# Kernel optimization log

Hardware: AMD Instinct MI355X
Metric: run time of the kernel (lower is better)

## Reference

```python
import jax, jax.numpy as jnp
import numpy as np

B, S, V, D, H, DK, DH, L = 1, 2048, 256, 1024, 16, 64, 4096, 4
EPS = 1e-5
SCALE = 1.0 / np.sqrt(DK)


def _ln(x, g, b):
    mu = jnp.mean(x, axis=-1, keepdims=True)
    var = jnp.mean(jnp.square(x - mu), axis=-1, keepdims=True)
    return (x - mu) * jax.lax.rsqrt(var + EPS) * g + b


def setup_inputs() -> dict:
    key = jax.random.key(0)
    ks = jax.random.split(key, 20)
    f = lambda k, shape: (0.02 * jax.random.normal(k, shape)).astype(jnp.float32)
    return {
        "x": jax.random.randint(ks[0], (B, S), 0, V),
        "emb": f(ks[1], (V, D)),
        "pos": f(ks[2], (S, D)),
        "Wq": f(ks[3], (L, D, H * DK)), "bq": jnp.zeros((L, H * DK), jnp.float32),
        "Wk": f(ks[4], (L, D, H * DK)), "bk": jnp.zeros((L, H * DK), jnp.float32),
        "Wv": f(ks[5], (L, D, H * DK)), "bv": jnp.zeros((L, H * DK), jnp.float32),
        "Wo": f(ks[6], (L, H * DK, D)),
        "ln1_g": jnp.ones((L, D), jnp.float32), "ln1_b": jnp.zeros((L, D), jnp.float32),
        "W1": f(ks[7], (L, D, DH)), "b1": jnp.zeros((L, DH), jnp.float32),
        "W2": f(ks[8], (L, DH, D)), "b2": jnp.zeros((L, D), jnp.float32),
        "ln2_g": jnp.ones((L, D), jnp.float32), "ln2_b": jnp.zeros((L, D), jnp.float32),
        "head_w": f(ks[9], (D, V)), "head_b": jnp.zeros((V,), jnp.float32),
    }


def _forward(x, emb, pos, Wq, bq, Wk, bk, Wv, bv, Wo, ln1_g, ln1_b,
             W1, b1, W2, b2, ln2_g, ln2_b, head_w, head_b):
    h = emb[x] + pos[:S]                      # [B,S,D]
    causal = jnp.tril(jnp.ones((S, S), bool))  # additive -inf above diag
    for i in range(L):
        # --- naive attention: explicit QK^T, mask, softmax, @V ---
        q = (h @ Wq[i] + bq[i]).reshape(B, S, H, DK)
        k = (h @ Wk[i] + bk[i]).reshape(B, S, H, DK)
        v = (h @ Wv[i] + bv[i]).reshape(B, S, H, DK)
        scores = jnp.einsum('bqhd,bkhd->bhqk', q * SCALE, k)   # [B,H,S,S]
        scores = jnp.where(causal[None, None], scores, -jnp.inf)
        p = jax.nn.softmax(scores, axis=-1)
        a = jnp.einsum('bhqk,bkhd->bqhd', p, v).reshape(B, S, H * DK) @ Wo[i]
        # --- TransformerLayer: x + ln2(mlp(x + ln1(attn(x)))) ---
        u = h + _ln(a, ln1_g[i], ln1_b[i])
        m = jax.nn.gelu(u @ W1[i] + b1[i], approximate=False) @ W2[i] + b2[i]
        h = h + _ln(m, ln2_g[i], ln2_b[i])
    return h @ head_w + head_b                 # [B,S,V]


def reference(x, emb, pos, Wq, bq, Wk, bk, Wv, bv, Wo, ln1_g, ln1_b,
              W1, b1, W2, b2, ln2_g, ln2_b, head_w, head_b):
    return _forward(x, emb, pos, Wq, bq, Wk, bk, Wv, bv, Wo, ln1_g, ln1_b,
                    W1, b1, W2, b2, ln2_g, ln2_b, head_w, head_b)
```

## Files before the change

### kernel.cpp

```cpp
#include <hip/hip_runtime.h>
#include <hip/hip_bf16.h>
#include <cstdint>
#include <math.h>

static constexpr int S_  = 2048;
static constexpr int D_  = 1024;
static constexpr int H_  = 16;
static constexpr int DK_ = 64;
static constexpr int DH_ = 4096;
static constexpr int L_  = 4;
static constexpr int V_  = 256;
#define ATT_SCALE 0.125f

typedef __bf16 bf16;
typedef __bf16 bf16x8 __attribute__((ext_vector_type(8)));
typedef __bf16 bf16x4v __attribute__((ext_vector_type(4)));
typedef float  f32x4  __attribute__((ext_vector_type(4)));

__device__ __forceinline__ __attribute__((address_space(3))) void* to_lds(const void* p) {
  return (__attribute__((address_space(3))) void*)(uintptr_t)p;
}
__device__ __forceinline__ __attribute__((address_space(1))) void* to_glb(const void* p) {
  return (__attribute__((address_space(1))) void*)(uintptr_t)p;
}

template <int GELU_EPI>
__global__ __launch_bounds__(256) void gemm_bf16_kernel(
    const bf16* __restrict__ A, const bf16* __restrict__ Bt,
    const float* __restrict__ bias, float* __restrict__ Cf, bf16* __restrict__ Cb,
    int M, int N, int K)
{
  __shared__ __align__(16) bf16 sA[2][128 * 64];
  __shared__ __align__(16) bf16 sB[2][64 * 64];
  const int tid  = threadIdx.x;
  const int wave = tid >> 6;
  const int lane = tid & 63;
  const int l16  = lane & 15;
  const int quad = lane >> 4;
  const int bm = blockIdx.x * 128;
  const int bn = blockIdx.y * 64;
  const int wm = (wave & 1) * 64;
  const int wn = (wave >> 1) * 32;

  const int srow = tid >> 3;
  const int sc8  = (tid & 7) ^ (srow & 7);
  const bf16* gA = A  + (size_t)(bm + srow) * K + sc8 * 8;
  const bf16* gB = Bt + (size_t)(bn + srow) * K + sc8 * 8;

  const int swz = l16 & 7;

  f32x4 acc[4][2] = {};

#pragma unroll
  for (int u = 0; u < 4; ++u)
    __builtin_amdgcn_global_load_lds(to_glb(gA + (size_t)u * 32 * K),
                                     to_lds(&sA[0][u * 2048 + tid * 8]), 16, 0, 0);
#pragma unroll
  for (int u = 0; u < 2; ++u)
    __builtin_amdgcn_global_load_lds(to_glb(gB + (size_t)u * 32 * K),
                                     to_lds(&sB[0][u * 2048 + tid * 8]), 16, 0, 0);

  int cur = 0;
  for (int k0 = 0; k0 < K; k0 += 64, cur ^= 1) {
    if (k0 + 64 < K) {
      const int nb = cur ^ 1;
      const size_t ko = k0 + 64;
#pragma unroll
      for (int u = 0; u < 4; ++u)
        __builtin_amdgcn_global_load_lds(to_glb(gA + ko + (size_t)u * 32 * K),
                                         to_lds(&sA[nb][u * 2048 + tid * 8]), 16, 0, 0);
#pragma unroll
      for (int u = 0; u < 2; ++u)
        __builtin_amdgcn_global_load_lds(to_glb(gB + ko + (size_t)u * 32 * K),
                                         to_lds(&sB[nb][u * 2048 + tid * 8]), 16, 0, 0);
      asm volatile("s_waitcnt vmcnt(6)" ::: "memory");
    } else {
      asm volatile("s_waitcnt vmcnt(0)" ::: "memory");
    }
    __builtin_amdgcn_s_barrier();

    bf16x8 af[2][4], bfv[2][2];
#pragma unroll
    for (int kc = 0; kc < 2; ++kc) {
      const int c8 = ((kc * 4 + quad) ^ swz) * 8;
#pragma unroll
      for (int i = 0; i < 4; ++i)
        af[kc][i] = *(const bf16x8*)&sA[cur][(wm + i * 16 + l16) * 64 + c8];
#pragma unroll
      for (int j = 0; j < 2; ++j)
        bfv[kc][j] = *(const bf16x8*)&sB[cur][(wn + j * 16 + l16) * 64 + c8];
    }
    asm volatile("s_waitcnt lgkmcnt(0)" ::: "memory");
    __builtin_amdgcn_s_barrier();

#pragma unroll
    for (int kc = 0; kc < 2; ++kc)
#pragma unroll
      for (int i = 0; i < 4; ++i)
#pragma unroll
        for (int j = 0; j < 2; ++j)
          acc[i][j] = __builtin_amdgcn_mfma_f32_16x16x32_bf16(af[kc][i], bfv[kc][j], acc[i][j], 0, 0, 0);
  }

#pragma unroll
  for (int i = 0; i < 4; ++i) {
#pragma unroll
    for (int j = 0; j < 2; ++j) {
      const int col = bn + wn + j * 16 + l16;
      const float bz = bias ? bias[col] : 0.0f;
#pragma unroll
      for (int r = 0; r < 4; ++r) {
        const int row = bm + wm + i * 16 + quad * 4 + r;
        float v = acc[i][j][r] + bz;
        if (GELU_EPI) v = 0.5f * v * (1.0f + erff(v * 0.70710678118654752f));
        if (Cf) Cf[(size_t)row * N + col] = v;
        if (Cb) Cb[(size_t)row * N + col] = (bf16)v;
      }
    }
  }
}

__global__ __launch_bounds__(256) void transpose_cast_kernel(
    const float* __restrict__ in, bf16* __restrict__ out, int K, int N)
{
  __shared__ float t[32][33];
  const int k0 = blockIdx.y * 32;
  const int n0 = blockIdx.x * 32;
  const int tx = threadIdx.x & 31;
  const int ty = threadIdx.x >> 5;
#pragma unroll
  for (int i = 0; i < 32; i += 8)
    t[ty + i][tx] = in[(size_t)(k0 + ty + i) * N + (n0 + tx)];
  __syncthreads();
#pragma unroll
  for (int i = 0; i < 32; i += 8)
    out[(size_t)(n0 + ty + i) * K + (k0 + tx)] = (bf16)t[tx][ty + i];
}

__global__ __launch_bounds__(256) void transpose3_cast_kernel(
    const float* __restrict__ in0, const float* __restrict__ in1, const float* __restrict__ in2,
    bf16* __restrict__ out, int K, int N)
{
  const float* in = (blockIdx.z == 0) ? in0 : (blockIdx.z == 1) ? in1 : in2;
  bf16* o = out + (size_t)blockIdx.z * K * N;
  __shared__ float t[32][33];
  const int k0 = blockIdx.y * 32;
  const int n0 = blockIdx.x * 32;
  const int tx = threadIdx.x & 31;
  const int ty = threadIdx.x >> 5;
#pragma unroll
  for (int i = 0; i < 32; i += 8)
    t[ty + i][tx] = in[(size_t)(k0 + ty + i) * N + (n0 + tx)];
  __syncthreads();
#pragma unroll
  for (int i = 0; i < 32; i += 8)
    o[(size_t)(n0 + ty + i) * K + (k0 + tx)] = (bf16)t[tx][ty + i];
}

__global__ __launch_bounds__(256) void vtrans_kernel(
    const bf16* __restrict__ qkv, bf16* __restrict__ vT)
{
  __shared__ bf16 t[32][65];
  const int s0 = blockIdx.x * 32;
  const int head = blockIdx.y;
  const int sr = threadIdx.x >> 3, d8 = (threadIdx.x & 7) * 8;
  bf16x8 v = *(const bf16x8*)(qkv + (size_t)(s0 + sr) * (3 * D_) + 2 * D_ + head * DK_ + d8);
#pragma unroll
  for (int i = 0; i < 8; ++i) t[sr][d8 + i] = v[i];
  __syncthreads();
  const int dw = threadIdx.x >> 2, s4 = (threadIdx.x & 3) * 8;
  bf16x8 o;
#pragma unroll
  for (int i = 0; i < 8; ++i) o[i] = t[s4 + i][dw];
  *(bf16x8*)(vT + (size_t)head * DK_ * S_ + (size_t)dw * S_ + s0 + s4) = o;
}

__global__ __launch_bounds__(256) void embed_kernel(
    const int* __restrict__ x, const float* __restrict__ emb, const float* __restrict__ pos,
    float* __restrict__ hf, bf16* __restrict__ hb)
{
  const int s = blockIdx.x;
  const int d = threadIdx.x * 4;
  const int tok = x[s];
  const float4 e = *(const float4*)(emb + (size_t)tok * D_ + d);
  const float4 p = *(const float4*)(pos + (size_t)s * D_ + d);
  float4 o; o.x = e.x + p.x; o.y = e.y + p.y; o.z = e.z + p.z; o.w = e.w + p.w;
  *(float4*)(hf + (size_t)s * D_ + d) = o;
  bf16x4v ob = {(bf16)o.x, (bf16)o.y, (bf16)o.z, (bf16)o.w};
  *(bf16x4v*)(hb + (size_t)s * D_ + d) = ob;
}

__device__ __forceinline__ float wave_reduce_sum(float v) {
#pragma unroll
  for (int off = 32; off > 0; off >>= 1) v += __shfl_xor(v, off, 64);
  return v;
}

__global__ __launch_bounds__(256) void ln_add_kernel(
    const float* __restrict__ src, const float* __restrict__ resid,
    const float* __restrict__ g, const float* __restrict__ b,
    float* __restrict__ outf, bf16* __restrict__ outb)
{
  const int r = blockIdx.x;
  const int t = threadIdx.x;
  const float4 x = ((const float4*)(src + (size_t)r * D_))[t];
  float s  = x.x + x.y + x.z + x.w;
  float s2 = x.x * x.x + x.y * x.y + x.z * x.z + x.w * x.w;
  s  = wave_reduce_sum(s);
  s2 = wave_reduce_sum(s2);
  __shared__ float red[8];
  const int wave = t >> 6, lane = t & 63;
  if (lane == 0) { red[wave] = s; red[4 + wave] = s2; }
  __syncthreads();
  s  = red[0] + red[1] + red[2] + red[3];
  s2 = red[4] + red[5] + red[6] + red[7];
  const float mu  = s * (1.0f / 1024.0f);
  const float var = s2 * (1.0f / 1024.0f) - mu * mu;
  const float rs  = rsqrtf(var + 1e-5f);
  const float4 gv = ((const float4*)g)[t];
  const float4 bv = ((const float4*)b)[t];
  const float4 hv = ((const float4*)(resid + (size_t)r * D_))[t];
  const float o0 = hv.x + (x.x - mu) * rs * gv.x + bv.x;
  const float o1 = hv.y + (x.y - mu) * rs * gv.y + bv.y;
  const float o2 = hv.z + (x.z - mu) * rs * gv.z + bv.z;
  const float o3 = hv.w + (x.w - mu) * rs * gv.w + bv.w;
  if (outf) { float4 o4; o4.x = o0; o4.y = o1; o4.z = o2; o4.w = o3;
              ((float4*)(outf + (size_t)r * D_))[t] = o4; }
  if (outb) { bf16x4v ob = {(bf16)o0, (bf16)o1, (bf16)o2, (bf16)o3};
              ((bf16x4v*)(outb + (size_t)r * D_))[t] = ob; }
}

__global__ __launch_bounds__(256) void attn_mfma_kernel(
    const bf16* __restrict__ qkv, const bf16* __restrict__ vT, bf16* __restrict__ out)
{
  __shared__ __align__(16) bf16 sK[2][64 * 64];
  __shared__ __align__(16) bf16 sV[2][64 * 64];
  __shared__ __align__(16) bf16 sP[4][16 * 64];

  const int head = blockIdx.y;
  const int xb   = blockIdx.x;
  const int qIdx = (head & 8) ? (31 - xb) : xb;
  const int qb   = qIdx * 64;
  const int tid  = threadIdx.x;
  const int wave = tid >> 6, lane = tid & 63;
  const int l16  = lane & 15, quad = lane >> 4;
  const int swz  = l16 & 7;

  const size_t rstr = 3 * D_;
  const bf16* kbase = qkv + D_ + head * DK_;
  const bf16* vbase = vT + (size_t)head * DK_ * S_;

  const int srow   = tid >> 3;
  const int kchunk = (tid & 7) ^ (srow & 7);

  bf16x8 aq0, aq1;
  {
    const bf16* qrow = qkv + (size_t)(qb + wave * 16 + l16) * rstr + head * DK_ + quad * 8;
    bf16x8 t0 = *(const bf16x8*)(qrow);
    bf16x8 t1 = *(const bf16x8*)(qrow + 32);
#pragma unroll
    for (int i = 0; i < 8; ++i) {
      aq0[i] = (bf16)((float)t0[i] * ATT_SCALE);
      aq1[i] = (bf16)((float)t1[i] * ATT_SCALE);
    }
  }

  f32x4 oa[4] = {};
  float lsum[4] = {0.0f, 0.0f, 0.0f, 0.0f};
  const int qrow0 = qb + wave * 16 + quad * 4;
  const int jmax = qb + 63;

#pragma unroll
  for (int u = 0; u < 2; ++u) {
    const int r = u * 32 + srow;
    __builtin_amdgcn_global_load_lds(to_glb(kbase + (size_t)r * rstr + kchunk * 8),
                                     to_lds(&sK[0][u * 2048 + tid * 8]), 16, 0, 0);
    __builtin_amdgcn_global_load_lds(to_glb(vbase + (size_t)r * S_ + kchunk * 8),
                                     to_lds(&sV[0][u * 2048 + tid * 8]), 16, 0, 0);
  }

  int cur = 0;
  for (int j0 = 0; j0 <= jmax; j0 += 64, cur ^= 1) {
    if (j0 + 64 <= jmax) {
      const int nb = cur ^ 1;
      const int jn = j0 + 64;
#pragma unroll
      for (int u = 0; u < 2; ++u) {
        const int r = u * 32 + srow;
        __builtin_amdgcn_global_load_lds(to_glb(kbase + (size_t)(jn + r) * rstr + kchunk * 8),
                                         to_lds(&sK[nb][u * 2048 + tid * 8]), 16, 0, 0);
        __builtin_amdgcn_global_load_lds(to_glb(vbase + (size_t)r * S_ + jn + kchunk * 8),
                                         to_lds(&sV[nb][u * 2048 + tid * 8]), 16, 0, 0);
      }
      asm volatile("s_waitcnt vmcnt(4)" ::: "memory");
    } else {
      asm volatile("s_waitcnt vmcnt(0)" ::: "memory");
    }
    __builtin_amdgcn_s_barrier();

    f32x4 sc[4];
#pragma unroll
    for (int n = 0; n < 4; ++n) {
      const bf16* kr = &sK[cur][(n * 16 + l16) * 64];
      bf16x8 bk0 = *(const bf16x8*)(kr + ((quad    ) ^ swz) * 8);
      bf16x8 bk1 = *(const bf16x8*)(kr + ((quad + 4) ^ swz) * 8);
      f32x4 z = {};
      z = __builtin_amdgcn_mfma_f32_16x16x32_bf16(aq0, bk0, z, 0, 0, 0);
      z = __builtin_amdgcn_mfma_f32_16x16x32_bf16(aq1, bk1, z, 0, 0, 0);
      sc[n] = z;
    }
    bf16 pb[4][4];
#pragma unroll
    for (int n = 0; n < 4; ++n) {
      const int key = j0 + n * 16 + l16;
#pragma unroll
      for (int r = 0; r < 4; ++r) {
        const float p = (key <= qrow0 + r) ? __expf(sc[n][r]) : 0.0f;
        lsum[r] += p;
        pb[n][r] = (bf16)p;
      }
    }
    bf16* pw = &sP[wave][0];
    const int cb = l16 >> 3, co = l16 & 7;
#pragma unroll
    for (int n = 0; n < 4; ++n) {
#pragma unroll
      for (int r = 0; r < 4; ++r) {
        const int row = quad * 4 + r;
        const int ch = (2 * n + cb) ^ (row & 7);
        pw[row * 64 + ch * 8 + co] = pb[n][r];
      }
    }
    asm volatile("s_waitcnt lgkmcnt(0)" ::: "memory");
    __builtin_amdgcn_wave_barrier();
    bf16x8 ap0 = *(const bf16x8*)&pw[l16 * 64 + ((quad    ) ^ swz) * 8];
    bf16x8 ap1 = *(const bf16x8*)&pw[l16 * 64 + ((quad + 4) ^ swz) * 8];

#pragma unroll
    for (int n = 0; n < 4; ++n) {
      const bf16* vr = &sV[cur][(n * 16 + l16) * 64];
      bf16x8 bv0 = *(const bf16x8*)(vr + ((quad    ) ^ swz) * 8);
      bf16x8 bv1 = *(const bf16x8*)(vr + ((quad + 4) ^ swz) * 8);
      oa[n] = __builtin_amdgcn_mfma_f32_16x16x32_bf16(ap0, bv0, oa[n], 0, 0, 0);
      oa[n] = __builtin_amdgcn_mfma_f32_16x16x32_bf16(ap1, bv1, oa[n], 0, 0, 0);
    }
    asm volatile("s_waitcnt lgkmcnt(0)" ::: "memory");
    __builtin_amdgcn_s_barrier();
  }

#pragma unroll
  for (int r = 0; r < 4; ++r) {
#pragma unroll
    for (int off = 1; off <= 8; off <<= 1)
      lsum[r] += __shfl_xor(lsum[r], off, 64);
  }
#pragma unroll
  for (int r = 0; r < 4; ++r) {
    const float inv = 1.0f / lsum[r];
    const int qrow = qrow0 + r;
#pragma unroll
    for (int n = 0; n < 4; ++n)
      out[(size_t)qrow * D_ + head * DK_ + n * 16 + l16] = (bf16)(oa[n][r] * inv);
  }
}

__global__ __launch_bounds__(256) void pack3_kernel(
    const float* __restrict__ a, const float* __restrict__ b, const float* __restrict__ c,
    float* __restrict__ out)
{
  const int i = blockIdx.x * 256 + threadIdx.x;
  if (i < 1024) out[i] = a[i];
  else if (i < 2048) out[i] = b[i - 1024];
  else if (i < 3072) out[i] = c[i - 2048];
}

extern "C" void kernel_launch(void* const* d_in, const int* in_sizes, int n_in,
                              void* d_out, int out_size, void* d_ws, size_t ws_size,
                              hipStream_t stream)
{
  const int*   x     = (const int*)d_in[0];
  const float* emb   = (const float*)d_in[1];
  const float* pos   = (const float*)d_in[2];
  const float* Wq    = (const float*)d_in[3];
  const float* bq    = (const float*)d_in[4];
  const float* Wk    = (const float*)d_in[5];
  const float* bk    = (const float*)d_in[6];
  const float* Wv    = (const float*)d_in[7];
  const float* bv    = (const float*)d_in[8];
  const float* Wo    = (const float*)d_in[9];
  const float* ln1g  = (const float*)d_in[10];
  const float* ln1b  = (const float*)d_in[11];
  const float* W1    = (const float*)d_in[12];
  const float* b1    = (const float*)d_in[13];
  const float* W2    = (const float*)d_in[14];
  const float* b2    = (const float*)d_in[15];
  const float* ln2g  = (const float*)d_in[16];
  const float* ln2b  = (const float*)d_in[17];
  const float* headw = (const float*)d_in[18];
  const float* headb = (const float*)d_in[19];

  char* w = (char*)d_ws;
  float* h_f32   = (float*)w;  w += (size_t)S_ * D_ * 4;
  bf16*  h_b     = (bf16*)w;   w += (size_t)S_ * D_ * 2;
  bf16*  qkv_b   = (bf16*)w;   w += (size_t)S_ * 3 * D_ * 2;
  bf16*  attn_b  = (bf16*)w;   w += (size_t)S_ * D_ * 2;
  float* a_f32   = (float*)w;  w += (size_t)S_ * D_ * 4;
  bf16*  u_b     = (bf16*)w;   w += (size_t)S_ * D_ * 2;
  bf16*  mh_b    = (bf16*)w;   w += (size_t)S_ * DH_ * 2;
  float* m_f32   = (float*)w;  w += (size_t)S_ * D_ * 4;
  bf16*  qkvT    = (bf16*)w;   w += (size_t)3 * D_ * D_ * 2;
  bf16*  woT     = (bf16*)w;   w += (size_t)D_ * D_ * 2;
  bf16*  w1T     = (bf16*)w;   w += (size_t)DH_ * D_ * 2;
  bf16*  w2T     = (bf16*)w;   w += (size_t)D_ * DH_ * 2;
  bf16*  headT   = (bf16*)w;   w += (size_t)V_ * D_ * 2;
  float* qkvbias = (float*)w;  w += (size_t)3 * D_ * 4;
  bf16*  vT      = qkvT;

  embed_kernel<<<dim3(S_), dim3(256), 0, stream>>>(x, emb, pos, h_f32, h_b);
  transpose_cast_kernel<<<dim3(V_ / 32, D_ / 32), dim3(256), 0, stream>>>(headw, headT, D_, V_);

  for (int i = 0; i < L_; ++i) {
    const float* Wq_i = Wq + (size_t)i * D_ * D_;
    const float* Wk_i = Wk + (size_t)i * D_ * D_;
    const float* Wv_i = Wv + (size_t)i * D_ * D_;
    const float* Wo_i = Wo + (size_t)i * D_ * D_;
    const float* W1_i = W1 + (size_t)i * D_ * DH_;
    const float* W2_i = W2 + (size_t)i * DH_ * D_;

    transpose3_cast_kernel<<<dim3(D_ / 32, D_ / 32, 3), dim3(256), 0, stream>>>(
        Wq_i, Wk_i, Wv_i, qkvT, D_, D_);
    pack3_kernel<<<dim3(12), dim3(256), 0, stream>>>(bq + (size_t)i * D_, bk + (size_t)i * D_, bv + (size_t)i * D_, qkvbias);
    gemm_bf16_kernel<0><<<dim3(S_ / 128, 3 * D_ / 64), dim3(256), 0, stream>>>(
        h_b, qkvT, qkvbias, nullptr, qkv_b, S_, 3 * D_, D_);
    vtrans_kernel<<<dim3(S_ / 32, H_), dim3(256), 0, stream>>>(qkv_b, vT);
    attn_mfma_kernel<<<dim3(S_ / 64, H_), dim3(256), 0, stream>>>(qkv_b, vT, attn_b);
    transpose_cast_kernel<<<dim3(D_ / 32, D_ / 32), dim3(256), 0, stream>>>(Wo_i, woT, D_, D_);
    gemm_bf16_kernel<0><<<dim3(S_ / 128, D_ / 64), dim3(256), 0, stream>>>(
        attn_b, woT, nullptr, a_f32, nullptr, S_, D_, D_);
    ln_add_kernel<<<dim3(S_), dim3(256), 0, stream>>>(
        a_f32, h_f32, ln1g + (size_t)i * D_, ln1b + (size_t)i * D_, nullptr, u_b);
    transpose_cast_kernel<<<dim3(DH_ / 32, D_ / 32), dim3(256), 0, stream>>>(W1_i, w1T, D_, DH_);
    gemm_bf16_kernel<1><<<dim3(S_ / 128, DH_ / 64), dim3(256), 0, stream>>>(
        u_b, w1T, b1 + (size_t)i * DH_, nullptr, mh_b, S_, DH_, D_);
    transpose_cast_kernel<<<dim3(D_ / 32, DH_ / 32), dim3(256), 0, stream>>>(W2_i, w2T, DH_, D_);
    gemm_bf16_kernel<0><<<dim3(S_ / 128, D_ / 64), dim3(256), 0, stream>>>(
        mh_b, w2T, b2 + (size_t)i * D_, m_f32, nullptr, S_, D_, DH_);
    ln_add_kernel<<<dim3(S_), dim3(256), 0, stream>>>(
        m_f32, h_f32, ln2g + (size_t)i * D_, ln2b + (size_t)i * D_, h_f32, h_b);
  }

  gemm_bf16_kernel<0><<<dim3(S_ / 128, V_ / 64), dim3(256), 0, stream>>>(
      h_b, headT, headb, (float*)d_out, nullptr, S_, V_, D_);
}
```

Baseline: 855.3 us.

## Widen GEMM N-tiles to 128 and add split-K with reduction kernels

Turns the GEMM into a template over N-tile width and split-K factor. The MLP1, Wo and MLP2 GEMMs now use 128-wide N tiles, and Wo, MLP2 and the head GEMMs split K across blockIdx.z, writing fp32 partials into reused workspace buffers. Separate reduce kernels then sum the partials and add bias. The aim is to raise occupancy on small-output GEMMs and get more reuse per tile. In exchange it adds extra partial-sum memory traffic and more kernel launches.

```diff
diff --git a/kernel.cpp b/kernel.cpp
--- a/kernel.cpp
+++ b/kernel.cpp
@@ -24,45 +24,51 @@
   return (__attribute__((address_space(1))) void*)(uintptr_t)p;
 }
 
-template <int GELU_EPI>
-__global__ __launch_bounds__(256) void gemm_bf16_kernel(
+template <int TN, int SPLIT, int GELU_EPI>
+__device__ __forceinline__ void gemm_body(
     const bf16* __restrict__ A, const bf16* __restrict__ Bt,
     const float* __restrict__ bias, float* __restrict__ Cf, bf16* __restrict__ Cb,
+    float* __restrict__ P0, float* __restrict__ P1,
     int M, int N, int K)
 {
+  constexpr int BU = TN / 32;
+  constexpr int JN = TN / 32;
   __shared__ __align__(16) bf16 sA[2][128 * 64];
-  __shared__ __align__(16) bf16 sB[2][64 * 64];
+  __shared__ __align__(16) bf16 sB[2][TN * 64];
   const int tid  = threadIdx.x;
   const int wave = tid >> 6;
   const int lane = tid & 63;
   const int l16  = lane & 15;
   const int quad = lane >> 4;
   const int bm = blockIdx.x * 128;
-  const int bn = blockIdx.y * 64;
+  const int bn = blockIdx.y * TN;
   const int wm = (wave & 1) * 64;
-  const int wn = (wave >> 1) * 32;
+  const int wn = (wave >> 1) * (TN / 2);
+
+  const int KS = K / SPLIT;
+  const size_t kofs = (SPLIT > 1) ? (size_t)blockIdx.z * KS : 0;
 
   const int srow = tid >> 3;
   const int sc8  = (tid & 7) ^ (srow & 7);
-  const bf16* gA = A  + (size_t)(bm + srow) * K + sc8 * 8;
-  const bf16* gB = Bt + (size_t)(bn + srow) * K + sc8 * 8;
+  const bf16* gA = A  + (size_t)(bm + srow) * K + kofs + sc8 * 8;
+  const bf16* gB = Bt + (size_t)(bn + srow) * K + kofs + sc8 * 8;
 
   const int swz = l16 & 7;
 
-  f32x4 acc[4][2] = {};
+  f32x4 acc[4][JN] = {};
 
 #pragma unroll
   for (int u = 0; u < 4; ++u)
     __builtin_amdgcn_global_load_lds(to_glb(gA + (size_t)u * 32 * K),
                                      to_lds(&sA[0][u * 2048 + tid * 8]), 16, 0, 0);
 #pragma unroll
-  for (int u = 0; u < 2; ++u)
+  for (int u = 0; u < BU; ++u)
     __builtin_amdgcn_global_load_lds(to_glb(gB + (size_t)u * 32 * K),
                                      to_lds(&sB[0][u * 2048 + tid * 8]), 16, 0, 0);
 
   int cur = 0;
-  for (int k0 = 0; k0 < K; k0 += 64, cur ^= 1) {
-    if (k0 + 64 < K) {
+  for (int k0 = 0; k0 < KS; k0 += 64, cur ^= 1) {
+    if (k0 + 64 < KS) {
       const int nb = cur ^ 1;
       const size_t ko = k0 + 64;
 #pragma unroll
@@ -70,16 +76,17 @@
         __builtin_amdgcn_global_load_lds(to_glb(gA + ko + (size_t)u * 32 * K),
                                          to_lds(&sA[nb][u * 2048 + tid * 8]), 16, 0, 0);
 #pragma unroll
-      for (int u = 0; u < 2; ++u)
+      for (int u = 0; u < BU; ++u)
         __builtin_amdgcn_global_load_lds(to_glb(gB + ko + (size_t)u * 32 * K),
                                          to_lds(&sB[nb][u * 2048 + tid * 8]), 16, 0, 0);
-      asm volatile("s_waitcnt vmcnt(6)" ::: "memory");
+      if constexpr (BU == 4) asm volatile("s_waitcnt vmcnt(8)" ::: "memory");
+      else                   asm volatile("s_waitcnt vmcnt(6)" ::: "memory");
     } else {
       asm volatile("s_waitcnt vmcnt(0)" ::: "memory");
     }
     __builtin_amdgcn_s_barrier();
 
-    bf16x8 af[2][4], bfv[2][2];
+    bf16x8 af[2][4], bfv[2][JN];
 #pragma unroll
     for (int kc = 0; kc < 2; ++kc) {
       const int c8 = ((kc * 4 + quad) ^ swz) * 8;
@@ -87,7 +94,7 @@
       for (int i = 0; i < 4; ++i)
         af[kc][i] = *(const bf16x8*)&sA[cur][(wm + i * 16 + l16) * 64 + c8];
 #pragma unroll
-      for (int j = 0; j < 2; ++j)
+      for (int j = 0; j < JN; ++j)
         bfv[kc][j] = *(const bf16x8*)&sB[cur][(wn + j * 16 + l16) * 64 + c8];
     }
     asm volatile("s_waitcnt lgkmcnt(0)" ::: "memory");
@@ -98,27 +105,106 @@
 #pragma unroll
       for (int i = 0; i < 4; ++i)
 #pragma unroll
-        for (int j = 0; j < 2; ++j)
+        for (int j = 0; j < JN; ++j)
           acc[i][j] = __builtin_amdgcn_mfma_f32_16x16x32_bf16(af[kc][i], bfv[kc][j], acc[i][j], 0, 0, 0);
   }
 
-#pragma unroll
-  for (int i = 0; i < 4; ++i) {
-#pragma unroll
-    for (int j = 0; j < 2; ++j) {
-      const int col = bn + wn + j * 16 + l16;
-      const float bz = bias ? bias[col] : 0.0f;
-#pragma unroll
-      for (int r = 0; r < 4; ++r) {
-        const int row = bm + wm + i * 16 + quad * 4 + r;
-        float v = acc[i][j][r] + bz;
-        if (GELU_EPI) v = 0.5f * v * (1.0f + erff(v * 0.70710678118654752f));
-        if (Cf) Cf[(size_t)row * N + col] = v;
-        if (Cb) Cb[(size_t)row * N + col] = (bf16)v;
+  if constexpr (SPLIT > 1) {
+    float* Pf;
+    if constexpr (SPLIT == 4)
+      Pf = (blockIdx.z < 2) ? (P0 + (size_t)blockIdx.z * ((size_t)M * N))
+                            : (P1 + (size_t)(blockIdx.z - 2) * ((size_t)M * N));
+    else
+      Pf = P0 + (size_t)blockIdx.z * ((size_t)M * N);
+#pragma unroll
+    for (int i = 0; i < 4; ++i)
+#pragma unroll
+      for (int j = 0; j < JN; ++j) {
+        const int col = bn + wn + j * 16 + l16;
+#pragma unroll
+        for (int r = 0; r < 4; ++r) {
+          const int row = bm + wm + i * 16 + quad * 4 + r;
+          Pf[(size_t)row * N + col] = acc[i][j][r];
+        }
       }
-    }
-  }
-}
+  } else {
+#pragma unroll
+    for (int i = 0; i < 4; ++i) {
+#pragma unroll
+      for (int j = 0; j < JN; ++j) {
+        const int col = bn + wn + j * 16 + l16;
+        const float bz = bias ? bias[col] : 0.0f;
+#pragma unroll
+        for (int r = 0; r < 4; ++r) {
+          const int row = bm + wm + i * 16 + quad * 4 + r;
+          float v = acc[i][j][r] + bz;
+          if (GELU_EPI) v = 0.5f * v * (1.0f + erff(v * 0.70710678118654752f));
+          if (Cf) Cf[(size_t)row * N + col] = v;
+          if (Cb) Cb[(size_t)row * N + col] = (bf16)v;
+        }
+      }
+    }
+  }
+}
+
+__global__ __launch_bounds__(256) void gemm_qkv_kernel(
+    const bf16* __restrict__ A, const bf16* __restrict__ Bt,
+    const float* __restrict__ bias, bf16* __restrict__ Cb, int M, int N, int K)
+{ gemm_body<64, 1, 0>(A, Bt, bias, nullptr, Cb, nullptr, nullptr, M, N, K); }
+
+__global__ __launch_bounds__(256) void gemm_wo_kernel(
+    const bf16* __restrict__ A, const bf16* __restrict__ Bt,
+    float* __restrict__ P0, int M, int N, int K)
+{ gemm_body<128, 2, 0>(A, Bt, nullptr, nullptr, nullptr, P0, nullptr, M, N, K); }
+
+__global__ __launch_bounds__(256) void gemm_mlp1_kernel(
+    const bf16* __restrict__ A, const bf16* __restrict__ Bt,
+    const float* __restrict__ bias, bf16* __restrict__ Cb, int M, int N, int K)
+{ gemm_body<128, 1, 1>(A, Bt, bias, nullptr, Cb, nullptr, nullptr, M, N, K); }
+
+__global__ __launch_bounds__(256) void gemm_mlp2_kernel(
+    const bf16* __restrict__ A, const bf16* __restrict__ Bt,
+    float* __restrict__ P0, float* __restrict__ P1, int M, int N, int K)
+{ gemm_body<128, 4, 0>(A, Bt, nullptr, nullptr, nullptr, P0, P1, M, N, K); }
+
+__global__ __launch_bounds__(256) void gemm_head_kernel(
+    const bf16* __restrict__ A, const bf16* __restrict__ Bt,
+    float* __restrict__ P0, float* __restrict__ P1, int M, int N, int K)
+{ gemm_body<64, 4, 0>(A, Bt, nullptr, nullptr, nullptr, P0, P1, M, N, K); }
+
+template <int SPLIT>
+__device__ __forceinline__ void splitk_reduce_body(
+    const float* __restrict__ P0, const float* __restrict__ P1,
+    const float* __restrict__ bias, float* __restrict__ Cf,
+    size_t MN, int N)
+{
+  const size_t i = ((size_t)blockIdx.x * 256 + threadIdx.x) * 4;
+  const float4 a = *(const float4*)(P0 + i);
+  const float4 b = *(const float4*)(P0 + MN + i);
+  float4 o;
+  o.x = a.x + b.x; o.y = a.y + b.y; o.z = a.z + b.z; o.w = a.w + b.w;
+  if constexpr (SPLIT == 4) {
+    const float4 c = *(const float4*)(P1 + i);
+    const float4 d = *(const float4*)(P1 + MN + i);
+    o.x += c.x + d.x; o.y += c.y + d.y; o.z += c.z + d.z; o.w += c.w + d.w;
+  }
+  if (bias) {
+    const int col = (int)(i & (size_t)(N - 1));
+    const float4 bz = *(const float4*)(bias + col);
+    o.x += bz.x; o.y += bz.y; o.z += bz.z; o.w += bz.w;
+  }
+  *(float4*)(Cf + i) = o;
+}
+
+__global__ __launch_bounds__(256) void splitk_reduce2_kernel(
+    const float* __restrict__ P0, const float* __restrict__ bias,
+    float* __restrict__ Cf, size_t MN, int N)
+{ splitk_reduce_body<2>(P0, nullptr, bias, Cf, MN, N); }
+
+__global__ __launch_bounds__(256) void splitk_reduce4_kernel(
+    const float* __restrict__ P0, const float* __restrict__ P1,
+    const float* __restrict__ bias, float* __restrict__ Cf, size_t MN, int N)
+{ splitk_reduce_body<4>(P0, P1, bias, Cf, MN, N); }
 
 __global__ __launch_bounds__(256) void transpose_cast_kernel(
     const float* __restrict__ in, bf16* __restrict__ out, int K, int N)
@@ -416,6 +502,12 @@
   float* qkvbias = (float*)w;  w += (size_t)3 * D_ * 4;
   bf16*  vT      = qkvT;
 
+  float* woP  = (float*)u_b;
+  float* m2P0 = (float*)attn_b;
+  float* m2P1 = (float*)qkvT;
+  float* hP0  = (float*)attn_b;
+  float* hP1  = hP0 + 2 * (size_t)S_ * V_;
+
   embed_kernel<<<dim3(S_), dim3(256), 0, stream>>>(x, emb, pos, h_f32, h_b);
   transpose_cast_kernel<<<dim3(V_ / 32, D_ / 32), dim3(256), 0, stream>>>(headw, headT, D_, V_);
 
@@ -430,25 +522,31 @@
     transpose3_cast_kernel<<<dim3(D_ / 32, D_ / 32, 3), dim3(256), 0, stream>>>(
         Wq_i, Wk_i, Wv_i, qkvT, D_, D_);
     pack3_kernel<<<dim3(12), dim3(256), 0, stream>>>(bq + (size_t)i * D_, bk + (size_t)i * D_, bv + (size_t)i * D_, qkvbias);
-    gemm_bf16_kernel<0><<<dim3(S_ / 128, 3 * D_ / 64), dim3(256), 0, stream>>>(
-        h_b, qkvT, qkvbias, nullptr, qkv_b, S_, 3 * D_, D_);
+    gemm_qkv_kernel<<<dim3(S_ / 128, 3 * D_ / 64), dim3(256), 0, stream>>>(
+        h_b, qkvT, qkvbias, qkv_b, S_, 3 * D_, D_);
     vtrans_kernel<<<dim3(S_ / 32, H_), dim3(256), 0, stream>>>(qkv_b, vT);
     attn_mfma_kernel<<<dim3(S_ / 64, H_), dim3(256), 0, stream>>>(qkv_b, vT, attn_b);
     transpose_cast_kernel<<<dim3(D_ / 32, D_ / 32), dim3(256), 0, stream>>>(Wo_i, woT, D_, D_);
-    gemm_bf16_kernel<0><<<dim3(S_ / 128, D_ / 64), dim3(256), 0, stream>>>(
-        attn_b, woT, nullptr, a_f32, nullptr, S_, D_, D_);
+    gemm_wo_kernel<<<dim3(S_ / 128, D_ / 128, 2), dim3(256), 0, stream>>>(
+        attn_b, woT, woP, S_, D_, D_);
+    splitk_reduce2_kernel<<<dim3((unsigned)((size_t)S_ * D_ / 1024)), dim3(256), 0, stream>>>(
+        woP, nullptr, a_f32, (size_t)S_ * D_, D_);
     ln_add_kernel<<<dim3(S_), dim3(256), 0, stream>>>(
         a_f32, h_f32, ln1g + (size_t)i * D_, ln1b + (size_t)i * D_, nullptr, u_b);
     transpose_cast_kernel<<<dim3(DH_ / 32, D_ / 32), dim3(256), 0, stream>>>(W1_i, w1T, D_, DH_);
-    gemm_bf16_kernel<1><<<dim3(S_ / 128, DH_ / 64), dim3(256), 0, stream>>>(
-        u_b, w1T, b1 + (size_t)i * DH_, nullptr, mh_b, S_, DH_, D_);
+    gemm_mlp1_kernel<<<dim3(S_ / 128, DH_ / 128), dim3(256), 0, stream>>>(
+        u_b, w1T, b1 + (size_t)i * DH_, mh_b, S_, DH_, D_);
     transpose_cast_kernel<<<dim3(D_ / 32, DH_ / 32), dim3(256), 0, stream>>>(W2_i, w2T, DH_, D_);
-    gemm_bf16_kernel<0><<<dim3(S_ / 128, D_ / 64), dim3(256), 0, stream>>>(
-        mh_b, w2T, b2 + (size_t)i * D_, m_f32, nullptr, S_, D_, DH_);
+    gemm_mlp2_kernel<<<dim3(S_ / 128, D_ / 128, 4), dim3(256), 0, stream>>>(
+        mh_b, w2T, m2P0, m2P1, S_, D_, DH_);
+    splitk_reduce4_kernel<<<dim3((unsigned)((size_t)S_ * D_ / 1024)), dim3(256), 0, stream>>>(
+        m2P0, m2P1, b2 + (size_t)i * D_, m_f32, (size_t)S_ * D_, D_);
     ln_add_kernel<<<dim3(S_), dim3(256), 0, stream>>>(
         m_f32, h_f32, ln2g + (size_t)i * D_, ln2b + (size_t)i * D_, h_f32, h_b);
   }
 
-  gemm_bf16_kernel<0><<<dim3(S_ / 128, V_ / 64), dim3(256), 0, stream>>>(
-      h_b, headT, headb, (float*)d_out, nullptr, S_, V_, D_);
-}
+  gemm_head_kernel<<<dim3(S_ / 128, V_ / 64, 4), dim3(256), 0, stream>>>(
+      h_b, headT, hP0, hP1, S_, V_, D_);
+  splitk_reduce4_kernel<<<dim3((unsigned)((size_t)S_ * V_ / 1024)), dim3(256), 0, stream>>>(
+      hP0, hP1, headb, (float*)d_out, (size_t)S_ * V_, V_);
+}
```

Result: no change. 868.0 us (+1.5%).
